# Optimization experiments

Hardware: AMD Instinct MI355X
Metric: run time of the kernel (lower is better)

Reference implementation:

```python
import jax, jax.numpy as jnp
import numpy as np

B, N, C = 4, 2048, 2048
H = 16
D = C // H  # head dim = 128


def setup_inputs() -> dict:
    key = jax.random.key(0)
    ks = jax.random.split(key, 5)
    s = 1.0 / np.sqrt(C)
    x = jax.random.normal(ks[0], (B, N, C), dtype=jnp.float32)
    w_qkv = jax.random.normal(ks[1], (C, 3 * C), dtype=jnp.float32) * s
    b_qkv = jax.random.normal(ks[2], (3 * C,), dtype=jnp.float32) * 0.01
    w_proj = jax.random.normal(ks[3], (C, C), dtype=jnp.float32) * s
    b_proj = jax.random.normal(ks[4], (C,), dtype=jnp.float32) * 0.01
    return {"x": x, "w_qkv": w_qkv, "b_qkv": b_qkv, "w_proj": w_proj, "b_proj": b_proj}


def reference(x, w_qkv, b_qkv, w_proj, b_proj):
    scale = D ** (-0.5)
    qkv = x @ w_qkv + b_qkv                              # [B,N,3C]
    qkv = qkv.reshape(B, N, 3, H, D).transpose(2, 0, 3, 1, 4)  # [3,B,H,N,D]
    q, k, v = qkv[0], qkv[1], qkv[2]
    attn = jnp.einsum('bhnd,bhmd->bhnm', q, k) * scale   # [B,H,N,N]
    attn = jax.nn.softmax(attn, axis=-1)
    out = jnp.einsum('bhnm,bhmd->bhnd', attn, v)         # [B,H,N,D]
    out = out.transpose(0, 2, 1, 3).reshape(B, N, C)
    return out @ w_proj + b_proj
```

## Files before the change

### kernel.cpp

```cpp
#include <hip/hip_runtime.h>

typedef short bf16x8 __attribute__((ext_vector_type(8)));
typedef float f32x4 __attribute__((ext_vector_type(4)));
typedef float f32x16 __attribute__((ext_vector_type(16)));
typedef unsigned int u32x4 __attribute__((ext_vector_type(4)));
typedef unsigned short u16;
typedef unsigned int u32;

__device__ __forceinline__ u16 f2bf(float f) {
  unsigned u = __builtin_bit_cast(unsigned, f);
  u += 0x7fffu + ((u >> 16) & 1u);
  return (u16)(u >> 16);
}

__device__ __forceinline__ void async16(const void* g, void* l) {
  __builtin_amdgcn_global_load_lds(
      (const __attribute__((address_space(1))) void*)g,
      (__attribute__((address_space(3))) void*)l, 16, 0, 0);
}

__device__ __forceinline__ float fexp2(float x) {
#if __has_builtin(__builtin_amdgcn_exp2f)
  return __builtin_amdgcn_exp2f(x);
#else
  return exp2f(x);
#endif
}

__device__ __forceinline__ float max3f(float a, float b, float c) {
  return fmaxf(fmaxf(a, b), c);
}

__global__ __launch_bounds__(256) void k_cvt(const float* __restrict__ src,
                                             u16* __restrict__ dst, int n4) {
  int i = blockIdx.x * blockDim.x + threadIdx.x;
  int stride = gridDim.x * blockDim.x;
  for (; i < n4; i += stride) {
    float4 f = ((const float4*)src)[i];
    ushort4 o;
    o.x = f2bf(f.x); o.y = f2bf(f.y); o.z = f2bf(f.z); o.w = f2bf(f.w);
    ((ushort4*)dst)[i] = o;
  }
}

__global__ __launch_bounds__(256) void k_tcvt(const float* __restrict__ src,
                                              u16* __restrict__ dst,
                                              int R, int C) {
  __shared__ float tile[64][65];
  int c0 = blockIdx.x * 64, r0 = blockIdx.y * 64;
  int tx = threadIdx.x & 63, ty = threadIdx.x >> 6;
#pragma unroll
  for (int i = 0; i < 64; i += 4)
    tile[ty + i][tx] = src[(size_t)(r0 + ty + i) * C + c0 + tx];
  __syncthreads();
#pragma unroll
  for (int i = 0; i < 64; i += 4)
    dst[(size_t)(c0 + ty + i) * R + r0 + tx] = f2bf(tile[tx][ty + i]);
}


__device__ __forceinline__ void stage_tile(u16* lds, const u16* gsrc, int tid) {
  const int r0 = tid >> 3, sl = tid & 7;
#pragma unroll
  for (int h = 0; h < 2; h++)
#pragma unroll
    for (int cc = 0; cc < 2; cc++) {
      int row = r0 + cc * 64;
      async16(gsrc + (size_t)(h * 128 + row) * 2048 + ((sl ^ (row & 7)) << 3),
              (char*)lds + ((size_t)(h * 1024 + row * 8 + sl) << 4));
    }
}

template <int QM>
__device__ __forceinline__ void rd_a(bf16x8 (&dst)[4][2], const u16* base,
                                     int lo, int g) {
#pragma unroll
  for (int m2 = 0; m2 < 4; m2++)
#pragma unroll
    for (int ks = 0; ks < 2; ks++) {
      int row = QM * 64 + m2 * 16 + lo;
      dst[m2][ks] = *(const bf16x8*)((const char*)base + row * 128 +
                                     (((ks * 4 + g) ^ (row & 7)) << 4));
    }
}

template <int QN>
__device__ __forceinline__ void rd_b(bf16x8 (&dst)[2][2], const u16* base,
                                     int brow_base, int lo, int g) {
#pragma unroll
  for (int n2 = 0; n2 < 2; n2++)
#pragma unroll
    for (int ks = 0; ks < 2; ks++) {
      int row = brow_base + QN * 32 + n2 * 16 + lo;
      dst[n2][ks] = *(const bf16x8*)((const char*)base + row * 128 +
                                     (((ks * 4 + g) ^ (row & 7)) << 4));
    }
}

template <int QM, int QN>
__device__ __forceinline__ void do_mm(f32x4 (&acc)[8][4], bf16x8 (&fa)[4][2],
                                      bf16x8 (&fb)[2][2]) {
  __builtin_amdgcn_s_setprio(1);
#pragma unroll
  for (int m2 = 0; m2 < 4; m2++)
#pragma unroll
    for (int n2 = 0; n2 < 2; n2++)
#pragma unroll
      for (int ks = 0; ks < 2; ks++)
        acc[QM * 4 + m2][QN * 2 + n2] = __builtin_amdgcn_mfma_f32_16x16x32_bf16(
            fa[m2][ks], fb[n2][ks], acc[QM * 4 + m2][QN * 2 + n2], 0, 0, 0);
  __builtin_amdgcn_s_setprio(0);
}

template <int EPI, int NT>
__global__ __launch_bounds__(512, 2) void k_gemm(
    const u16* __restrict__ A, const u16* __restrict__ Bt,
    const float* __restrict__ bias,
    u16* __restrict__ qb, u16* __restrict__ kb, u16* __restrict__ vtb,
    float* __restrict__ fout) {
  __shared__ u16 aL[2][2][128 * 64];
  __shared__ u16 bL[2][2][128 * 64];
  const int tid = threadIdx.x;
  const int lane = tid & 63, w = tid >> 6;
  const int lo = lane & 15, g = lane >> 4;
  const int wm = w >> 2, wn = w & 3;
  const int brow_base = (wn & 1) * 64;
  const int nwg = NT * 32;
  const int swz = (blockIdx.x & 7) * (nwg >> 3) + (blockIdx.x >> 3);
  const int by = swz / NT, bx = swz % NT;
  const int rm0 = by * 256, cn0 = bx * 256;
  const u16* Ab = A + (size_t)rm0 * 2048;
  const u16* Bb = Bt + (size_t)cn0 * 2048;

  f32x4 acc[8][4];
#pragma unroll
  for (int i = 0; i < 8; i++)
#pragma unroll
    for (int j = 0; j < 4; j++) {
      acc[i][j][0] = 0.f; acc[i][j][1] = 0.f;
      acc[i][j][2] = 0.f; acc[i][j][3] = 0.f;
    }

  stage_tile(&aL[0][0][0], Ab, tid);
  stage_tile(&bL[0][0][0], Bb, tid);

  for (int it = 0; it < 16; ++it) {
#pragma unroll
    for (int tt = 0; tt < 2; ++tt) {
      const int tn = 2 * it + tt + 1;
      const u16* aS = &aL[tt][wm][0];
      const u16* bS = &bL[tt][wn >> 1][0];
      bf16x8 fa[4][2], fb0[2][2], fb1[2][2];
      if (tn < 32) {
        stage_tile(&aL[tt ^ 1][0][0], Ab + tn * 64, tid);
        asm volatile("s_waitcnt vmcnt(4)" ::: "memory");
      } else {
        asm volatile("s_waitcnt vmcnt(0)" ::: "memory");
      }
      __builtin_amdgcn_s_barrier();
      rd_a<0>(fa, aS, lo, g);
      rd_b<0>(fb0, bS, brow_base, lo, g);
      asm volatile("s_waitcnt lgkmcnt(0)" ::: "memory");
      do_mm<0, 0>(acc, fa, fb0);
      rd_b<1>(fb1, bS, brow_base, lo, g);
      asm volatile("s_waitcnt lgkmcnt(0)" ::: "memory");
      do_mm<0, 1>(acc, fa, fb1);
      if (tn < 32) stage_tile(&bL[tt ^ 1][0][0], Bb + tn * 64, tid);
      rd_a<1>(fa, aS, lo, g);
      asm volatile("s_waitcnt lgkmcnt(0)" ::: "memory");
      do_mm<1, 1>(acc, fa, fb1);
      do_mm<1, 0>(acc, fa, fb0);
      __builtin_amdgcn_s_barrier();
    }
  }

#pragma unroll
  for (int qi = 0; qi < 8; qi++) {
    const int rowb = rm0 + wm * 128 + (qi >> 2) * 64 + (qi & 3) * 16 + g * 4;
#pragma unroll
    for (int nj = 0; nj < 4; nj++) {
      const int col = cn0 + wn * 64 + (nj >> 1) * 32 + (nj & 1) * 16 + lo;
      const float bcol = bias[col];
      const float v0 = acc[qi][nj][0] + bcol, v1 = acc[qi][nj][1] + bcol;
      const float v2 = acc[qi][nj][2] + bcol, v3 = acc[qi][nj][3] + bcol;
      if constexpr (EPI == 0) {
        const int which = col >> 11;
        const int hc = col & 2047, d = hc & 127;
        const int bh = ((rowb >> 11) << 4) | (hc >> 7);
        if (which == 2) {
          ushort4 us;
          us.x = f2bf(v0); us.y = f2bf(v1); us.z = f2bf(v2); us.w = f2bf(v3);
          *(ushort4*)(vtb + (size_t)bh * 262144 + (size_t)d * 2048 +
                      (rowb & 2047)) = us;
        } else {
          u16* dst = (which == 0) ? qb : kb;
          const float sc = (which == 0) ? 0.12751743f : 1.0f;
          size_t base = (size_t)bh * 262144 + (size_t)(rowb & 2047) * 128 + d;
          dst[base] = f2bf(v0 * sc);
          dst[base + 128] = f2bf(v1 * sc);
          dst[base + 256] = f2bf(v2 * sc);
          dst[base + 384] = f2bf(v3 * sc);
        }
      } else {
        fout[(size_t)(rowb + 0) * 2048 + col] = v0;
        fout[(size_t)(rowb + 1) * 2048 + col] = v1;
        fout[(size_t)(rowb + 2) * 2048 + col] = v2;
        fout[(size_t)(rowb + 3) * 2048 + col] = v3;
      }
    }
  }
}

__global__ __launch_bounds__(512) void k_attn(
    const u16* __restrict__ qg, const u16* __restrict__ kg,
    const u16* __restrict__ vtg, u16* __restrict__ og) {
  __shared__ u16 kt[2][64 * 128];
  __shared__ u16 vt[2][128 * 64];
  const int bh = blockIdx.x;
  const int b = bh >> 4, h = bh & 15;
  const u16* Q = qg + (size_t)bh * 262144;
  const u16* Kp = kg + (size_t)bh * 262144;
  const u16* VT = vtg + (size_t)bh * 262144;
  const int tid = threadIdx.x;
  const int lane = tid & 63, w = tid >> 6;
  const int ql = lane & 31, hi = lane >> 5;
  const int q0 = blockIdx.y * 256 + w * 32;

  const int c0 = tid, c1 = tid + 512;
  const int kva = c0 >> 4, ksa = c0 & 15, kvb = c1 >> 4, ksb = c1 & 15;
  const size_t koff_a = (size_t)kva * 128 + (size_t)((ksa ^ (kva & 7)) * 8);
  const size_t koff_b = (size_t)kvb * 128 + (size_t)((ksb ^ (kvb & 7)) * 8);
  const int da = c0 >> 3, sva = c0 & 7, db = c1 >> 3, svb = c1 & 7;
  const size_t voff_a = (size_t)da * 2048 + (size_t)((sva ^ (da & 7)) * 8);
  const size_t voff_b = (size_t)db * 2048 + (size_t)((svb ^ (db & 7)) * 8);

  bf16x8 qf[8];
#pragma unroll
  for (int c = 0; c < 8; c++)
    qf[c] = *(const bf16x8*)(Q + (size_t)(q0 + ql) * 128 + c * 16 + hi * 8);

  f32x16 o[4];
#pragma unroll
  for (int nd = 0; nd < 4; nd++)
#pragma unroll
    for (int r = 0; r < 16; r++) o[nd][r] = 0.f;
  float m = -1e30f, l = 0.f;

  {
    async16(Kp + koff_a, &kt[0][c0 * 8]);
    async16(Kp + koff_b, &kt[0][c1 * 8]);
    async16(VT + voff_a, &vt[0][c0 * 8]);
    async16(VT + voff_b, &vt[0][c1 * 8]);
  }
  int cur = 0;
  for (int kv0 = 0; kv0 < 2048; kv0 += 64) {
    __syncthreads();
    if (kv0 + 64 < 2048) {
      const u16* kbp = Kp + (size_t)(kv0 + 64) * 128;
      const u16* vbp = VT + (kv0 + 64);
      int nx = cur ^ 1;
      async16(kbp + koff_a, &kt[nx][c0 * 8]);
      async16(kbp + koff_b, &kt[nx][c1 * 8]);
      async16(vbp + voff_a, &vt[nx][c0 * 8]);
      async16(vbp + voff_b, &vt[nx][c1 * 8]);
    }
    const char* ktb = (const char*)&kt[cur][0];
    const char* vtb = (const char*)&vt[cur][0];

    f32x16 sacc[2];
#pragma unroll
    for (int s2 = 0; s2 < 2; s2++)
#pragma unroll
      for (int r = 0; r < 16; r++) sacc[s2][r] = 0.f;
    __builtin_amdgcn_s_setprio(1);
#pragma unroll
    for (int c = 0; c < 8; c++)
#pragma unroll
      for (int s2 = 0; s2 < 2; s2++) {
        int kv = s2 * 32 + ql;
        int phys = kv * 256 + ((c * 32 + hi * 16) ^ ((kv & 7) << 4));
        bf16x8 kf = *(const bf16x8*)(ktb + phys);
        sacc[s2] = __builtin_amdgcn_mfma_f32_32x32x16_bf16(kf, qf[c], sacc[s2], 0, 0, 0);
      }
    __builtin_amdgcn_s_setprio(0);

    float t0 = max3f(sacc[0][0], sacc[0][1], sacc[0][2]);
    float t1 = max3f(sacc[0][3], sacc[0][4], sacc[0][5]);
    float t2 = max3f(sacc[0][6], sacc[0][7], sacc[0][8]);
    float t3 = max3f(sacc[0][9], sacc[0][10], sacc[0][11]);
    float t4 = max3f(sacc[0][12], sacc[0][13], sacc[0][14]);
    float t5 = max3f(sacc[0][15], sacc[1][0], sacc[1][1]);
    float t6 = max3f(sacc[1][2], sacc[1][3], sacc[1][4]);
    float t7 = max3f(sacc[1][5], sacc[1][6], sacc[1][7]);
    float t8 = max3f(sacc[1][8], sacc[1][9], sacc[1][10]);
    float t9 = max3f(sacc[1][11], sacc[1][12], sacc[1][13]);
    float ta = fmaxf(sacc[1][14], sacc[1][15]);
    t0 = max3f(t0, t1, t2); t3 = max3f(t3, t4, t5);
    t6 = max3f(t6, t7, t8); t9 = max3f(t9, ta, t0);
    float tm = max3f(t3, t6, t9);
    tm = fmaxf(tm, __shfl_xor(tm, 32));
    if (!__all(tm <= m)) {
      float mnew = fmaxf(m, tm);
      float corr = fexp2(m - mnew);
      l *= corr;
#pragma unroll
      for (int nd = 0; nd < 4; nd++)
#pragma unroll
        for (int r = 0; r < 16; r++) o[nd][r] *= corr;
      m = mnew;
    }
    float ps0 = 0.f, ps1 = 0.f, ps2 = 0.f, ps3 = 0.f;
#pragma unroll
    for (int s2 = 0; s2 < 2; s2++)
#pragma unroll
      for (int r = 0; r < 16; r++) {
        float p = fexp2(sacc[s2][r] - m);
        sacc[s2][r] = p;
        if (s2 == 0 && r < 8) ps0 += p;
        else if (s2 == 0) ps1 += p;
        else if (r < 8) ps2 += p;
        else ps3 += p;
      }
    l += (ps0 + ps1) + (ps2 + ps3);

    bf16x8 pf[4];
#pragma unroll
    for (int s2 = 0; s2 < 2; s2++) {
      u32 pk[8];
#pragma unroll
      for (int i = 0; i < 8; i++) {
        u32 t;
        asm("v_cvt_pk_bf16_f32 %0, %1, %2"
            : "=v"(t) : "v"(sacc[s2][2 * i]), "v"(sacc[s2][2 * i + 1]));
        pk[i] = t;
      }
#pragma unroll
      for (int ksl = 0; ksl < 2; ksl++) {
        u32 a0 = pk[4 * ksl + 0], b0 = pk[4 * ksl + 2];
        u32 a1 = pk[4 * ksl + 1], b1 = pk[4 * ksl + 3];
        asm("v_permlane32_swap_b32 %0, %1" : "+v"(a0), "+v"(b0));
        asm("v_permlane32_swap_b32 %0, %1" : "+v"(a1), "+v"(b1));
        u32x4 fr = {a0, a1, b0, b1};
        pf[s2 * 2 + ksl] = __builtin_bit_cast(bf16x8, fr);
      }
    }

    __builtin_amdgcn_s_setprio(1);
#pragma unroll
    for (int nd = 0; nd < 4; nd++)
#pragma unroll
      for (int ks = 0; ks < 4; ks++) {
        int d = nd * 32 + ql;
        int phys = d * 128 + ((ks * 32 + hi * 16) ^ ((d & 7) << 4));
        bf16x8 vf = *(const bf16x8*)(vtb + phys);
        o[nd] = __builtin_amdgcn_mfma_f32_32x32x16_bf16(vf, pf[ks], o[nd], 0, 0, 0);
      }
    __builtin_amdgcn_s_setprio(0);
    cur ^= 1;
  }

  float lt = l + __shfl_xor(l, 32);
  float inv = 1.0f / lt;
  size_t rowbase = ((size_t)(b * 2048 + q0 + ql)) * 2048 + h * 128 + hi * 4;
#pragma unroll
  for (int nd = 0; nd < 4; nd++)
#pragma unroll
    for (int j2 = 0; j2 < 4; j2++) {
      ushort4 us;
      us.x = f2bf(o[nd][4 * j2 + 0] * inv);
      us.y = f2bf(o[nd][4 * j2 + 1] * inv);
      us.z = f2bf(o[nd][4 * j2 + 2] * inv);
      us.w = f2bf(o[nd][4 * j2 + 3] * inv);
      *(ushort4*)(og + rowbase + nd * 32 + j2 * 8) = us;
    }
}

extern "C" void kernel_launch(void* const* d_in, const int* in_sizes, int n_in,
                              void* d_out, int out_size, void* d_ws, size_t ws_size,
                              hipStream_t stream) {
  const float* x      = (const float*)d_in[0];
  const float* w_qkv  = (const float*)d_in[1];
  const float* b_qkv  = (const float*)d_in[2];
  const float* w_proj = (const float*)d_in[3];
  const float* b_proj = (const float*)d_in[4];
  float* out = (float*)d_out;

  char* p = (char*)d_ws;
  u16* xb     = (u16*)p; p += (size_t)8192 * 2048 * 2;
  u16* wqkvT  = (u16*)p; p += (size_t)6144 * 2048 * 2;
  u16* wprojT = (u16*)p; p += (size_t)2048 * 2048 * 2;
  u16* qb     = (u16*)p; p += (size_t)64 * 2048 * 128 * 2;
  u16* kb     = (u16*)p; p += (size_t)64 * 2048 * 128 * 2;
  u16* vtb    = (u16*)p; p += (size_t)64 * 2048 * 128 * 2;

  k_cvt<<<2048, 256, 0, stream>>>(x, xb, (8192 * 2048) / 4);
  k_tcvt<<<dim3(6144 / 64, 2048 / 64), 256, 0, stream>>>(w_qkv, wqkvT, 2048, 6144);
  k_tcvt<<<dim3(2048 / 64, 2048 / 64), 256, 0, stream>>>(w_proj, wprojT, 2048, 2048);
  k_gemm<0, 24><<<768, 512, 0, stream>>>(xb, wqkvT, b_qkv, qb, kb, vtb, nullptr);
  k_attn<<<dim3(64, 8), 512, 0, stream>>>(qb, kb, vtb, xb);
  k_gemm<1, 8><<<256, 512, 0, stream>>>(xb, wprojT, b_proj, nullptr, nullptr, nullptr, out);
}
```

Measured before the change: 446.6 us.

## Shrink GEMM block tile from 256x256 to 128x128 with 4 waves

Reworks the GEMM kernel to use 128x128 output tiles with 256 threads (4 waves, each 64x64) instead of 256x256 tiles with 512 threads. LDS staging, fragment reads, accumulator layout, epilogue indexing and grid sizes are adjusted to match. The aim is more workgroups and better occupancy and load balance across CUs, especially for the projection GEMM that previously launched only 256 blocks. The cost is lower arithmetic intensity per tile, so global and LDS traffic per FLOP roughly doubles.

```diff
diff --git a/kernel.cpp b/kernel.cpp
--- a/kernel.cpp
+++ b/kernel.cpp
@@ -65,20 +65,19 @@
   for (int h = 0; h < 2; h++)
 #pragma unroll
     for (int cc = 0; cc < 2; cc++) {
-      int row = r0 + cc * 64;
-      async16(gsrc + (size_t)(h * 128 + row) * 2048 + ((sl ^ (row & 7)) << 3),
-              (char*)lds + ((size_t)(h * 1024 + row * 8 + sl) << 4));
-    }
-}
-
-template <int QM>
+      int row = r0 + cc * 32;
+      async16(gsrc + (size_t)(h * 64 + row) * 2048 + ((sl ^ (row & 7)) << 3),
+              (char*)lds + ((size_t)(h * 512 + row * 8 + sl) << 4));
+    }
+}
+
 __device__ __forceinline__ void rd_a(bf16x8 (&dst)[4][2], const u16* base,
                                      int lo, int g) {
 #pragma unroll
   for (int m2 = 0; m2 < 4; m2++)
 #pragma unroll
     for (int ks = 0; ks < 2; ks++) {
-      int row = QM * 64 + m2 * 16 + lo;
+      int row = m2 * 16 + lo;
       dst[m2][ks] = *(const bf16x8*)((const char*)base + row * 128 +
                                      (((ks * 4 + g) ^ (row & 7)) << 4));
     }
@@ -86,19 +85,19 @@
 
 template <int QN>
 __device__ __forceinline__ void rd_b(bf16x8 (&dst)[2][2], const u16* base,
-                                     int brow_base, int lo, int g) {
+                                     int lo, int g) {
 #pragma unroll
   for (int n2 = 0; n2 < 2; n2++)
 #pragma unroll
     for (int ks = 0; ks < 2; ks++) {
-      int row = brow_base + QN * 32 + n2 * 16 + lo;
+      int row = QN * 32 + n2 * 16 + lo;
       dst[n2][ks] = *(const bf16x8*)((const char*)base + row * 128 +
                                      (((ks * 4 + g) ^ (row & 7)) << 4));
     }
 }
 
-template <int QM, int QN>
-__device__ __forceinline__ void do_mm(f32x4 (&acc)[8][4], bf16x8 (&fa)[4][2],
+template <int QN>
+__device__ __forceinline__ void do_mm(f32x4 (&acc)[4][4], bf16x8 (&fa)[4][2],
                                       bf16x8 (&fb)[2][2]) {
   __builtin_amdgcn_s_setprio(1);
 #pragma unroll
@@ -107,34 +106,33 @@
     for (int n2 = 0; n2 < 2; n2++)
 #pragma unroll
       for (int ks = 0; ks < 2; ks++)
-        acc[QM * 4 + m2][QN * 2 + n2] = __builtin_amdgcn_mfma_f32_16x16x32_bf16(
-            fa[m2][ks], fb[n2][ks], acc[QM * 4 + m2][QN * 2 + n2], 0, 0, 0);
+        acc[m2][QN * 2 + n2] = __builtin_amdgcn_mfma_f32_16x16x32_bf16(
+            fa[m2][ks], fb[n2][ks], acc[m2][QN * 2 + n2], 0, 0, 0);
   __builtin_amdgcn_s_setprio(0);
 }
 
 template <int EPI, int NT>
-__global__ __launch_bounds__(512, 2) void k_gemm(
+__global__ __launch_bounds__(256, 2) void k_gemm(
     const u16* __restrict__ A, const u16* __restrict__ Bt,
     const float* __restrict__ bias,
     u16* __restrict__ qb, u16* __restrict__ kb, u16* __restrict__ vtb,
     float* __restrict__ fout) {
-  __shared__ u16 aL[2][2][128 * 64];
-  __shared__ u16 bL[2][2][128 * 64];
+  __shared__ u16 aL[2][2][64 * 64];
+  __shared__ u16 bL[2][2][64 * 64];
   const int tid = threadIdx.x;
   const int lane = tid & 63, w = tid >> 6;
   const int lo = lane & 15, g = lane >> 4;
-  const int wm = w >> 2, wn = w & 3;
-  const int brow_base = (wn & 1) * 64;
-  const int nwg = NT * 32;
+  const int wm = w >> 1, wn = w & 1;
+  const int nwg = 64 * NT;
   const int swz = (blockIdx.x & 7) * (nwg >> 3) + (blockIdx.x >> 3);
   const int by = swz / NT, bx = swz % NT;
-  const int rm0 = by * 256, cn0 = bx * 256;
+  const int rm0 = by * 128, cn0 = bx * 128;
   const u16* Ab = A + (size_t)rm0 * 2048;
   const u16* Bb = Bt + (size_t)cn0 * 2048;
 
-  f32x4 acc[8][4];
-#pragma unroll
-  for (int i = 0; i < 8; i++)
+  f32x4 acc[4][4];
+#pragma unroll
+  for (int i = 0; i < 4; i++)
 #pragma unroll
     for (int j = 0; j < 4; j++) {
       acc[i][j][0] = 0.f; acc[i][j][1] = 0.f;
@@ -149,7 +147,7 @@
     for (int tt = 0; tt < 2; ++tt) {
       const int tn = 2 * it + tt + 1;
       const u16* aS = &aL[tt][wm][0];
-      const u16* bS = &bL[tt][wn >> 1][0];
+      const u16* bS = &bL[tt][wn][0];
       bf16x8 fa[4][2], fb0[2][2], fb1[2][2];
       if (tn < 32) {
         stage_tile(&aL[tt ^ 1][0][0], Ab + tn * 64, tid);
@@ -158,28 +156,24 @@
         asm volatile("s_waitcnt vmcnt(0)" ::: "memory");
       }
       __builtin_amdgcn_s_barrier();
-      rd_a<0>(fa, aS, lo, g);
-      rd_b<0>(fb0, bS, brow_base, lo, g);
+      rd_a(fa, aS, lo, g);
+      rd_b<0>(fb0, bS, lo, g);
       asm volatile("s_waitcnt lgkmcnt(0)" ::: "memory");
-      do_mm<0, 0>(acc, fa, fb0);
-      rd_b<1>(fb1, bS, brow_base, lo, g);
+      do_mm<0>(acc, fa, fb0);
+      if (tn < 32) stage_tile(&bL[tt ^ 1][0][0], Bb + tn * 64, tid);
+      rd_b<1>(fb1, bS, lo, g);
       asm volatile("s_waitcnt lgkmcnt(0)" ::: "memory");
-      do_mm<0, 1>(acc, fa, fb1);
-      if (tn < 32) stage_tile(&bL[tt ^ 1][0][0], Bb + tn * 64, tid);
-      rd_a<1>(fa, aS, lo, g);
-      asm volatile("s_waitcnt lgkmcnt(0)" ::: "memory");
-      do_mm<1, 1>(acc, fa, fb1);
-      do_mm<1, 0>(acc, fa, fb0);
+      do_mm<1>(acc, fa, fb1);
       __builtin_amdgcn_s_barrier();
     }
   }
 
 #pragma unroll
-  for (int qi = 0; qi < 8; qi++) {
-    const int rowb = rm0 + wm * 128 + (qi >> 2) * 64 + (qi & 3) * 16 + g * 4;
+  for (int qi = 0; qi < 4; qi++) {
+    const int rowb = rm0 + wm * 64 + qi * 16 + g * 4;
 #pragma unroll
     for (int nj = 0; nj < 4; nj++) {
-      const int col = cn0 + wn * 64 + (nj >> 1) * 32 + (nj & 1) * 16 + lo;
+      const int col = cn0 + wn * 64 + nj * 16 + lo;
       const float bcol = bias[col];
       const float v0 = acc[qi][nj][0] + bcol, v1 = acc[qi][nj][1] + bcol;
       const float v2 = acc[qi][nj][2] + bcol, v3 = acc[qi][nj][3] + bcol;
@@ -396,7 +390,7 @@
   k_cvt<<<2048, 256, 0, stream>>>(x, xb, (8192 * 2048) / 4);
   k_tcvt<<<dim3(6144 / 64, 2048 / 64), 256, 0, stream>>>(w_qkv, wqkvT, 2048, 6144);
   k_tcvt<<<dim3(2048 / 64, 2048 / 64), 256, 0, stream>>>(w_proj, wprojT, 2048, 2048);
-  k_gemm<0, 24><<<768, 512, 0, stream>>>(xb, wqkvT, b_qkv, qb, kb, vtb, nullptr);
+  k_gemm<0, 48><<<3072, 256, 0, stream>>>(xb, wqkvT, b_qkv, qb, kb, vtb, nullptr);
   k_attn<<<dim3(64, 8), 512, 0, stream>>>(qb, kb, vtb, xb);
-  k_gemm<1, 8><<<256, 512, 0, stream>>>(xb, wprojT, b_proj, nullptr, nullptr, nullptr, out);
-}
+  k_gemm<1, 16><<<1024, 256, 0, stream>>>(xb, wprojT, b_proj, nullptr, nullptr, nullptr, out);
+}
```

Result: slower. 518.5 us (+16.1%).
